# Performance work log

Hardware: AMD Instinct MI355X
Metric: run time of the kernel (lower is better)

Reference implementation:

```python
import jax, jax.numpy as jnp
import numpy as np

CLIP_LEN = 8      # == num_frame
NUM_NODES = 7     # == group_size
NUM_BASIC = 1024
NUM_MIXED = 8192
T = 2 * CLIP_LEN - 1          # 15 temporal offsets
N = 1 + NUM_NODES * CLIP_LEN  # 57 graph size


def setup_inputs() -> dict:
    key = jax.random.key(0)
    k1, k2, k3, k4 = jax.random.split(key, 4)
    mat = jax.random.normal(k1, (NUM_BASIC, NUM_NODES, NUM_NODES), dtype=jnp.float32)
    temp_extent = jax.random.normal(k2, (NUM_BASIC, T), dtype=jnp.float32)
    # nn.Linear(num_basic, num_mixed): weight [out,in], bias [out]
    W = jax.random.normal(k3, (NUM_MIXED, NUM_BASIC), dtype=jnp.float32) * (1.0 / np.sqrt(NUM_BASIC))
    b = jax.random.normal(k4, (NUM_MIXED,), dtype=jnp.float32) * 0.01
    return {"mat": mat, "temp_extent": temp_extent, "W": W, "b": b}


def reference(mat, temp_extent, W, b):
    n, cl = NUM_NODES, CLIP_LEN
    Hb = mat.shape[0]
    te = jax.nn.sigmoid(temp_extent) + 1.0                      # [Hb, T]
    x = jnp.einsum('ht,hnm->htmn', te, mat)                     # [Hb, T, n, n]
    x = jax.nn.relu(x)
    x = jnp.transpose(x, (1, 2, 3, 0)).reshape(T * n, n, Hb)    # (t m) n h
    y = x @ W.T + b                                             # [(t m), n, Hm]
    y = jax.nn.relu(jnp.transpose(y, (2, 1, 0)))                # [Hm, n, T*n]
    Hm = y.shape[0]
    # vectorized version of the per-frame slice-write loop:
    # frame i reads cols n*(cl-1-i) : n*(2*cl-1-i) of y
    starts = n * (cl - 1 - jnp.arange(cl))                      # [cl]
    idx = starts[:, None] + jnp.arange(n * cl)[None, :]         # [cl, n*cl]
    blocks = y[:, :, idx]                                       # [Hm, n, cl, n*cl]
    blocks = jnp.transpose(blocks, (0, 2, 1, 3)).reshape(Hm, n * cl, n * cl)
    base = jnp.zeros((Hm, N, N), dtype=y.dtype)
    base = base.at[:, 0::7, 0::7].set(1.0)                      # person-node anchors
    mixed = base.at[:, 1:, 1:].set(blocks)                      # [Hm, N, N]
    # degree normalization D^{-1/2} A D^{-1/2} (row sums, clamped at 1)
    d = jnp.clip(mixed.sum(axis=2), 1.0, None) ** -0.5          # [Hm, N]
    ret = d[:, :, None] * mixed * d[:, None, :]
    return ret
```

## Files before the change

### kernel.cpp

```cpp
#include <hip/hip_runtime.h>
#include <hip/hip_bf16.h>

#define HB 1024
#define HM 8192
#define NR 735
#define NPAD 768
#define NOUT 57
#define KSPLIT 2

typedef __attribute__((ext_vector_type(8))) _Float16 half8;
typedef __attribute__((ext_vector_type(4))) _Float16 half4v;
typedef __attribute__((ext_vector_type(4))) float floatx4;

__global__ __launch_bounds__(256) void prep_x2_kernel(
    const float* __restrict__ mat, const float* __restrict__ tex,
    _Float16* __restrict__ Xh) {
  const int r = blockIdx.x;
  const int n = r % 7;
  const int tm = r / 7;
  const int m = tm % 7;
  const int t = tm / 7;
#pragma unroll
  for (int i = 0; i < 4; ++i) {
    const int h = i * 256 + threadIdx.x;
    float v = 0.f;
    if (r < NR) {
      const float mv = mat[h * 49 + n * 7 + m];
      const float te = 1.f / (1.f + expf(-tex[h * 15 + t])) + 1.f;
      v = te * mv;
      v = v > 0.f ? v : 0.f;
    }
    Xh[r * HB + h] = (_Float16)v;
  }
}

__global__ __launch_bounds__(256) void prep_w_kernel(
    const float4* __restrict__ W, half4v* __restrict__ Wh) {
  const int idx = blockIdx.x * 256 + threadIdx.x;
  const float4 v = W[idx];
  half4v h;
  h.x = (_Float16)v.x;
  h.y = (_Float16)v.y;
  h.z = (_Float16)v.z;
  h.w = (_Float16)v.w;
  Wh[idx] = h;
}

__global__ __launch_bounds__(256, 3) void gemm_kernel(
    const _Float16* __restrict__ A,
    const _Float16* __restrict__ B,
    float* __restrict__ Yp) {
  __shared__ __align__(16) _Float16 As[128 * 32];
  __shared__ __align__(16) _Float16 Bs[128 * 32];

  const int tid = threadIdx.x;
  const int lane = tid & 63;
  const int wave = tid >> 6;
  const int bn = blockIdx.x;
  const int bm = blockIdx.y;
  const int ks = blockIdx.z;
  const int wm = (wave >> 1) * 64;
  const int wn = (wave & 1) * 64;

  floatx4 acc[4][4] = {};

  const int srow = lane >> 2;
  const int skh = (lane & 3) * 8;
  const size_t abase = (size_t)(bm * 128) * HB;
  const size_t bbase = (size_t)(bn * 128) * HB;

  const int mrow = lane & 15;
  const int quad = lane >> 4;

  const int kbeg = ks * (HB / KSPLIT);
  const int kend = kbeg + (HB / KSPLIT);
  for (int k0 = kbeg; k0 < kend; k0 += 32) {
#pragma unroll
    for (int it = 0; it < 2; ++it) {
      const int chunk = wave * 2 + it;
      const int row = chunk * 16 + srow;
      __builtin_amdgcn_global_load_lds(
          (const __attribute__((address_space(1))) void*)(A + abase + (size_t)row * HB + k0 + skh),
          (__attribute__((address_space(3))) void*)(As + chunk * 512), 16, 0, 0);
      __builtin_amdgcn_global_load_lds(
          (const __attribute__((address_space(1))) void*)(B + bbase + (size_t)row * HB + k0 + skh),
          (__attribute__((address_space(3))) void*)(Bs + chunk * 512), 16, 0, 0);
    }
    __syncthreads();

    half8 af[4], bf[4];
#pragma unroll
    for (int i = 0; i < 4; ++i) {
      af[i] = *(const half8*)(As + (wm + i * 16 + mrow) * 32 + quad * 8);
      bf[i] = *(const half8*)(Bs + (wn + i * 16 + mrow) * 32 + quad * 8);
    }
#pragma unroll
    for (int i = 0; i < 4; ++i)
#pragma unroll
      for (int j = 0; j < 4; ++j)
        acc[i][j] = __builtin_amdgcn_mfma_f32_16x16x32_f16(af[i], bf[j], acc[i][j], 0, 0, 0);
    __syncthreads();
  }

  float* Yk = Yp + (size_t)ks * HM * NPAD;
#pragma unroll
  for (int i = 0; i < 4; ++i) {
#pragma unroll
    for (int j = 0; j < 4; ++j) {
#pragma unroll
      for (int reg = 0; reg < 4; ++reg) {
        const int grow = bm * 128 + wm + i * 16 + quad * 4 + reg;
        const int gcol = bn * 128 + wn + j * 16 + mrow;
        Yk[(size_t)grow * NPAD + gcol] = acc[i][j][reg];
      }
    }
  }
}

__global__ __launch_bounds__(256) void epilogue_kernel(
    const float* __restrict__ Yp, const float* __restrict__ bias,
    float* __restrict__ out) {
  const int j = blockIdx.x;
  __shared__ float ly[NR];
  __shared__ float dd[NOUT];

  const float* y0 = Yp + (size_t)j * NPAD;
  const float* y1 = Yp + (size_t)(HM + j) * NPAD;
  const float bj = bias[j];
  for (int i = threadIdx.x; i < NR; i += 256) {
    float v = y0[i] + y1[i] + bj;
    ly[i] = v > 0.f ? v : 0.f;
  }
  __syncthreads();

  if (threadIdx.x < NOUT) {
    const int r = threadIdx.x;
    float s;
    if (r == 0) {
      s = 9.f;
    } else {
      const int c = (r - 1) / 7;
      const int n = (r - 1) % 7;
      const int base = 7 * (7 - c);
      s = (n == 6) ? 1.f : 0.f;
#pragma unroll
      for (int p = 0; p < 56; ++p) s += ly[(base + p) * 7 + n];
    }
    s = s < 1.f ? 1.f : s;
    dd[r] = rsqrtf(s);
  }
  __syncthreads();

  float* oj = out + (size_t)j * (NOUT * NOUT);
  for (int i = threadIdx.x; i < NOUT * NOUT; i += 256) {
    const int r = i / NOUT;
    const int q = i % NOUT;
    float v;
    if (r == 0) {
      v = (q % 7 == 0) ? dd[0] * dd[q] : 0.f;
    } else {
      const int c = (r - 1) / 7;
      const int n = (r - 1) % 7;
      if (q == 0)
        v = (n == 6) ? dd[r] * dd[0] : 0.f;
      else
        v = dd[r] * ly[(7 * (7 - c) + q - 1) * 7 + n] * dd[q];
    }
    oj[i] = v;
  }
}

extern "C" void kernel_launch(void* const* d_in, const int* in_sizes, int n_in,
                              void* d_out, int out_size, void* d_ws, size_t ws_size,
                              hipStream_t stream) {
  const float* mat = (const float*)d_in[0];
  const float* tex = (const float*)d_in[1];
  const float* W = (const float*)d_in[2];
  const float* b = (const float*)d_in[3];
  float* out = (float*)d_out;

  char* ws = (char*)d_ws;
  _Float16* Xh = (_Float16*)(ws);
  _Float16* Wh = (_Float16*)(ws + (size_t)NPAD * HB * 2);
  float* Yp = (float*)(ws + (size_t)NPAD * HB * 2 + (size_t)HM * HB * 2);

  prep_x2_kernel<<<NPAD, 256, 0, stream>>>(mat, tex, Xh);
  prep_w_kernel<<<HM * HB / 4 / 256, 256, 0, stream>>>((const float4*)W, (half4v*)Wh);
  gemm_kernel<<<dim3(NPAD / 128, HM / 128, KSPLIT), 256, 0, stream>>>(Wh, Xh, Yp);
  epilogue_kernel<<<HM, 256, 0, stream>>>(Yp, b, out);
}
```

Measured before the change: 188.3 us.

## Fuse W fp16 conversion into GEMM, store fp16 partials, batch epilogue rows

Removes the separate W fp32->fp16 conversion kernel. The GEMM now loads fp32 W directly through registers, converts it, and writes it to LDS, which saves a full round trip of the fp16 W copy. Split-K partial results are stored in fp16 to halve partial-sum traffic. The epilogue now processes 4 output matrices per block and writes float4 stores. The trade-offs are that the A tile now goes through synchronous register loads instead of direct-to-LDS loads, W is re-read as fp32 by each of the 6 N-tile blocks, and fp16 partials lose precision.

```diff
diff --git a/kernel.cpp b/kernel.cpp
--- a/kernel.cpp
+++ b/kernel.cpp
@@ -7,6 +7,8 @@
 #define NPAD 768
 #define NOUT 57
 #define KSPLIT 2
+#define JB 4
+#define YS 737
 
 typedef __attribute__((ext_vector_type(8))) _Float16 half8;
 typedef __attribute__((ext_vector_type(4))) _Float16 half4v;
@@ -34,22 +36,10 @@
   }
 }
 
-__global__ __launch_bounds__(256) void prep_w_kernel(
-    const float4* __restrict__ W, half4v* __restrict__ Wh) {
-  const int idx = blockIdx.x * 256 + threadIdx.x;
-  const float4 v = W[idx];
-  half4v h;
-  h.x = (_Float16)v.x;
-  h.y = (_Float16)v.y;
-  h.z = (_Float16)v.z;
-  h.w = (_Float16)v.w;
-  Wh[idx] = h;
-}
-
 __global__ __launch_bounds__(256, 3) void gemm_kernel(
-    const _Float16* __restrict__ A,
-    const _Float16* __restrict__ B,
-    float* __restrict__ Yp) {
+    const float* __restrict__ W,
+    const _Float16* __restrict__ Xh,
+    _Float16* __restrict__ Yp) {
   __shared__ __align__(16) _Float16 As[128 * 32];
   __shared__ __align__(16) _Float16 Bs[128 * 32];
 
@@ -64,27 +54,38 @@
 
   floatx4 acc[4][4] = {};
 
-  const int srow = lane >> 2;
-  const int skh = (lane & 3) * 8;
-  const size_t abase = (size_t)(bm * 128) * HB;
+  const int brow = lane >> 2;
+  const int bkh = (lane & 3) * 8;
   const size_t bbase = (size_t)(bn * 128) * HB;
+
+  const int arow = tid >> 3;
+  const int acol = (tid & 7) * 4;
+  const float* const Wbase = W + (size_t)(bm * 128) * HB;
 
   const int mrow = lane & 15;
   const int quad = lane >> 4;
 
   const int kbeg = ks * (HB / KSPLIT);
-  const int kend = kbeg + (HB / KSPLIT);
-  for (int k0 = kbeg; k0 < kend; k0 += 32) {
+  for (int kk = 0; kk < HB / KSPLIT; kk += 32) {
+    const int k0 = kbeg + kk;
 #pragma unroll
     for (int it = 0; it < 2; ++it) {
       const int chunk = wave * 2 + it;
-      const int row = chunk * 16 + srow;
       __builtin_amdgcn_global_load_lds(
-          (const __attribute__((address_space(1))) void*)(A + abase + (size_t)row * HB + k0 + skh),
-          (__attribute__((address_space(3))) void*)(As + chunk * 512), 16, 0, 0);
-      __builtin_amdgcn_global_load_lds(
-          (const __attribute__((address_space(1))) void*)(B + bbase + (size_t)row * HB + k0 + skh),
+          (const __attribute__((address_space(1))) void*)(
+              Xh + bbase + (size_t)(chunk * 16 + brow) * HB + k0 + bkh),
           (__attribute__((address_space(3))) void*)(Bs + chunk * 512), 16, 0, 0);
+    }
+#pragma unroll
+    for (int it = 0; it < 4; ++it) {
+      const int r = it * 32 + arow;
+      const float4 w4 = *(const float4*)(Wbase + (size_t)r * HB + k0 + acol);
+      half4v h4;
+      h4.x = (_Float16)w4.x;
+      h4.y = (_Float16)w4.y;
+      h4.z = (_Float16)w4.z;
+      h4.w = (_Float16)w4.w;
+      *(half4v*)(As + r * 32 + acol) = h4;
     }
     __syncthreads();
 
@@ -102,7 +103,7 @@
     __syncthreads();
   }
 
-  float* Yk = Yp + (size_t)ks * HM * NPAD;
+  _Float16* const Yk = Yp + (size_t)ks * HM * NPAD;
 #pragma unroll
   for (int i = 0; i < 4; ++i) {
 #pragma unroll
@@ -111,30 +112,35 @@
       for (int reg = 0; reg < 4; ++reg) {
         const int grow = bm * 128 + wm + i * 16 + quad * 4 + reg;
         const int gcol = bn * 128 + wn + j * 16 + mrow;
-        Yk[(size_t)grow * NPAD + gcol] = acc[i][j][reg];
+        Yk[(size_t)grow * NPAD + gcol] = (_Float16)acc[i][j][reg];
       }
     }
   }
 }
 
 __global__ __launch_bounds__(256) void epilogue_kernel(
-    const float* __restrict__ Yp, const float* __restrict__ bias,
+    const _Float16* __restrict__ Yp, const float* __restrict__ bias,
     float* __restrict__ out) {
-  const int j = blockIdx.x;
-  __shared__ float ly[NR];
-  __shared__ float dd[NOUT];
-
-  const float* y0 = Yp + (size_t)j * NPAD;
-  const float* y1 = Yp + (size_t)(HM + j) * NPAD;
-  const float bj = bias[j];
-  for (int i = threadIdx.x; i < NR; i += 256) {
-    float v = y0[i] + y1[i] + bj;
-    ly[i] = v > 0.f ? v : 0.f;
+  const int tid = threadIdx.x;
+  const int j0 = blockIdx.x * JB;
+  __shared__ float ly[JB][YS];
+  __shared__ float dd[JB][NOUT];
+
+#pragma unroll
+  for (int jj = 0; jj < JB; ++jj) {
+    const _Float16* y0 = Yp + (size_t)(j0 + jj) * NPAD;
+    const _Float16* y1 = Yp + (size_t)(HM + j0 + jj) * NPAD;
+    const float bj = bias[j0 + jj];
+    for (int i = tid; i < NR; i += 256) {
+      float v = (float)y0[i] + (float)y1[i] + bj;
+      ly[jj][i] = v > 0.f ? v : 0.f;
+    }
   }
   __syncthreads();
 
-  if (threadIdx.x < NOUT) {
-    const int r = threadIdx.x;
+  if (tid < JB * NOUT) {
+    const int jj = tid / NOUT;
+    const int r = tid % NOUT;
     float s;
     if (r == 0) {
       s = 9.f;
@@ -144,29 +150,37 @@
       const int base = 7 * (7 - c);
       s = (n == 6) ? 1.f : 0.f;
 #pragma unroll
-      for (int p = 0; p < 56; ++p) s += ly[(base + p) * 7 + n];
+      for (int p = 0; p < 56; ++p) s += ly[jj][(base + p) * 7 + n];
     }
     s = s < 1.f ? 1.f : s;
-    dd[r] = rsqrtf(s);
+    dd[jj][r] = rsqrtf(s);
   }
   __syncthreads();
 
-  float* oj = out + (size_t)j * (NOUT * NOUT);
-  for (int i = threadIdx.x; i < NOUT * NOUT; i += 256) {
-    const int r = i / NOUT;
-    const int q = i % NOUT;
-    float v;
-    if (r == 0) {
-      v = (q % 7 == 0) ? dd[0] * dd[q] : 0.f;
-    } else {
-      const int c = (r - 1) / 7;
-      const int n = (r - 1) % 7;
-      if (q == 0)
-        v = (n == 6) ? dd[r] * dd[0] : 0.f;
-      else
-        v = dd[r] * ly[(7 * (7 - c) + q - 1) * 7 + n] * dd[q];
-    }
-    oj[i] = v;
+  float4* const o4 = (float4*)(out + (size_t)j0 * (NOUT * NOUT));
+  for (int idx = tid; idx < NOUT * NOUT; idx += 256) {
+    float4 v4;
+#pragma unroll
+    for (int e = 0; e < 4; ++e) {
+      const int g = idx * 4 + e;
+      const int jj = g / (NOUT * NOUT);
+      const int i = g % (NOUT * NOUT);
+      const int r = i / NOUT;
+      const int q = i % NOUT;
+      float v;
+      if (r == 0) {
+        v = (q % 7 == 0) ? dd[jj][0] * dd[jj][q] : 0.f;
+      } else {
+        const int c = (r - 1) / 7;
+        const int n = (r - 1) % 7;
+        if (q == 0)
+          v = (n == 6) ? dd[jj][r] * dd[jj][0] : 0.f;
+        else
+          v = dd[jj][r] * ly[jj][(7 * (7 - c) + q - 1) * 7 + n] * dd[jj][q];
+      }
+      ((float*)&v4)[e] = v;
+    }
+    o4[idx] = v4;
   }
 }
 
@@ -180,12 +194,10 @@
   float* out = (float*)d_out;
 
   char* ws = (char*)d_ws;
-  _Float16* Xh = (_Float16*)(ws);
-  _Float16* Wh = (_Float16*)(ws + (size_t)NPAD * HB * 2);
-  float* Yp = (float*)(ws + (size_t)NPAD * HB * 2 + (size_t)HM * HB * 2);
+  _Float16* Xh = (_Float16*)ws;
+  _Float16* Yp = (_Float16*)(ws + (size_t)NPAD * HB * 2);
 
   prep_x2_kernel<<<NPAD, 256, 0, stream>>>(mat, tex, Xh);
-  prep_w_kernel<<<HM * HB / 4 / 256, 256, 0, stream>>>((const float4*)W, (half4v*)Wh);
-  gemm_kernel<<<dim3(NPAD / 128, HM / 128, KSPLIT), 256, 0, stream>>>(Wh, Xh, Yp);
-  epilogue_kernel<<<HM, 256, 0, stream>>>(Yp, b, out);
-}
+  gemm_kernel<<<dim3(NPAD / 128, HM / 128, KSPLIT), 256, 0, stream>>>(W, Xh, Yp);
+  epilogue_kernel<<<HM / JB, 256, 0, stream>>>(Yp, b, out);
+}
```

Result: slower. 194.0 us (+3.0%).
